# Kernel tuning notes

Measured on AMD Instinct MI355X. Metric: run time of the kernel, lower is better.

## Reference

```python
import jax, jax.numpy as jnp
import numpy as np

# Stand-in base model config (HF-style causal LM)
L, D, H, DFF, V, T = 2, 1024, 16, 4096, 32000, 2
HD = D // H
B, S = 2, 1024


def setup_inputs() -> dict:
    key = jax.random.key(0)
    ks = jax.random.split(key, 20)
    s = 0.02
    ds = 0.002  # task-vector deltas are small finetuning differences
    inp = {
        "input_ids": jax.random.randint(ks[0], (B, S), 0, V, dtype=jnp.int32),
        "labels": jax.random.randint(ks[1], (B, S), 0, V, dtype=jnp.int32),
        "lambdas": jax.random.uniform(ks[2], (T,), jnp.float32) * 0.5,
        # base parameters (frozen, like base_model)
        "emb": jax.random.normal(ks[3], (V, D), jnp.float32) * s,
        "Wqkv": jax.random.normal(ks[4], (L, D, 3 * D), jnp.float32) * s,
        "Wo": jax.random.normal(ks[5], (L, D, D), jnp.float32) * s,
        "W1": jax.random.normal(ks[6], (L, D, DFF), jnp.float32) * s,
        "W2": jax.random.normal(ks[7], (L, DFF, D), jnp.float32) * s,
        "g1": jnp.ones((L, D), jnp.float32),
        "g2": jnp.ones((L, D), jnp.float32),
        "gf": jnp.ones((D,), jnp.float32),
        # stacked task-vector deltas: leading dim T (one slice per CPUStoredTaskVector)
        "d_emb": jax.random.normal(ks[8], (T, V, D), jnp.float32) * ds,
        "d_Wqkv": jax.random.normal(ks[9], (T, L, D, 3 * D), jnp.float32) * ds,
        "d_Wo": jax.random.normal(ks[10], (T, L, D, D), jnp.float32) * ds,
        "d_W1": jax.random.normal(ks[11], (T, L, D, DFF), jnp.float32) * ds,
        "d_W2": jax.random.normal(ks[12], (T, L, DFF, D), jnp.float32) * ds,
        "d_g1": jax.random.normal(ks[13], (T, L, D), jnp.float32) * ds,
        "d_g2": jax.random.normal(ks[14], (T, L, D), jnp.float32) * ds,
        "d_gf": jax.random.normal(ks[15], (T, D), jnp.float32) * ds,
    }
    return inp


def _ln(x, g):
    mu = x.mean(-1, keepdims=True)
    var = ((x - mu) ** 2).mean(-1, keepdims=True)
    return (x - mu) * jax.lax.rsqrt(var + 1e-5) * g


def reference(input_ids, labels, lambdas, emb, Wqkv, Wo, W1, W2, g1, g2, gf,
              d_emb, d_Wqkv, d_Wo, d_W1, d_W2, d_g1, d_g2, d_gf):
    # fused layerwise merge: param + sum_i lambdas[i] * delta_i (single pass over all deltas)
    m = lambda base, d: base + jnp.einsum("t,t...->...", lambdas, d)
    emb_m = m(emb, d_emb)
    x = emb_m[input_ids]  # [B, S, D]
    b, s, _ = x.shape
    causal = jnp.tril(jnp.ones((s, s), bool))

    def body(h, p):
        wqkv, wo, w1, w2, gg1, gg2 = p
        a = _ln(h, gg1)
        qkv = a @ wqkv  # [B,S,3D]
        q, k, v = jnp.split(qkv, 3, axis=-1)
        q = q.reshape(b, s, H, HD)
        k = k.reshape(b, s, H, HD)
        v = v.reshape(b, s, H, HD)
        att = jnp.einsum("bqhd,bkhd->bhqk", q, k) / jnp.sqrt(jnp.float32(HD))
        att = jnp.where(causal, att, jnp.float32(-1e9))
        att = jax.nn.softmax(att, axis=-1)
        o = jnp.einsum("bhqk,bkhd->bqhd", att, v).reshape(b, s, D)
        h = h + o @ wo
        a = _ln(h, gg2)
        h = h + jax.nn.gelu(a @ w1) @ w2
        return h, None

    merged = (m(Wqkv, d_Wqkv), m(Wo, d_Wo), m(W1, d_W1), m(W2, d_W2),
              m(g1, d_g1), m(g2, d_g2))
    x, _ = jax.lax.scan(body, x, merged)
    x = _ln(x, m(gf, d_gf))
    logits = x @ emb_m.T  # tied embeddings, [B,S,V]
    # HF causal-LM loss: shift logits left, labels right
    logp = jax.nn.log_softmax(logits[:, :-1, :], axis=-1)
    tgt = labels[:, 1:]
    nll = -jnp.take_along_axis(logp, tgt[..., None].astype(jnp.int32), axis=-1)[..., 0]
    return nll.mean()
```

## Files before the change

### kernel.cpp

```cpp
#include <hip/hip_runtime.h>
#include <math.h>

#define L_ 2
#define D_ 1024
#define H_ 16
#define HD_ 64
#define DFF_ 4096
#define V_ 32000
#define B_ 2
#define S_ 1024
#define BS_ (B_*S_)
#define D3_ (3*D_)
#define VC_ 6400

typedef __attribute__((ext_vector_type(8))) short short8;
typedef __attribute__((ext_vector_type(4))) float f32x4;

__device__ __forceinline__ float b2f(unsigned short u) {
    return __uint_as_float(((unsigned int)u) << 16);
}
__device__ __forceinline__ unsigned short f2b(float f) {
    unsigned int u = __float_as_uint(f);
    return (unsigned short)((u + 0x7fffu + ((u >> 16) & 1u)) >> 16);
}
__device__ __forceinline__ float blo(unsigned int u) { return __uint_as_float(u << 16); }
__device__ __forceinline__ float bhi(unsigned int u) { return __uint_as_float(u & 0xffff0000u); }

__device__ __forceinline__ void gld16(const void* g, void* l) {
    __builtin_amdgcn_global_load_lds(
        (const __attribute__((address_space(1))) unsigned int*)g,
        (__attribute__((address_space(3))) unsigned int*)l, 16, 0, 0);
}


__global__ void merge_f32_kernel(const float* __restrict__ base, const float* __restrict__ dlt,
                                 size_t tstride, const float* __restrict__ lam,
                                 float* __restrict__ out, int n) {
    float l0 = lam[0], l1 = lam[1];
    for (int i = blockIdx.x * blockDim.x + threadIdx.x; i < n; i += gridDim.x * blockDim.x)
        out[i] = base[i] + l0 * dlt[i] + l1 * dlt[i + tstride];
}

__global__ void merge_bf16_kernel(const float* __restrict__ base, const float* __restrict__ dlt,
                                  size_t tstride, const float* __restrict__ lam,
                                  unsigned short* __restrict__ out, size_t n4) {
    float l0 = lam[0], l1 = lam[1];
    for (size_t q = blockIdx.x * blockDim.x + threadIdx.x; q < n4; q += (size_t)gridDim.x * blockDim.x) {
        size_t i = q * 4;
        float4 b = *(const float4*)(base + i);
        float4 d0 = *(const float4*)(dlt + i);
        float4 d1 = *(const float4*)(dlt + tstride + i);
        ushort4 o;
        o.x = f2b(b.x + l0 * d0.x + l1 * d1.x);
        o.y = f2b(b.y + l0 * d0.y + l1 * d1.y);
        o.z = f2b(b.z + l0 * d0.z + l1 * d1.z);
        o.w = f2b(b.w + l0 * d0.w + l1 * d1.w);
        *(ushort4*)(out + i) = o;
    }
}

__global__ __launch_bounds__(256) void mt_kernel(const float* __restrict__ in,
                                                 const float* __restrict__ din, size_t tstride,
                                                 const float* __restrict__ lam,
                                                 unsigned short* __restrict__ outT,
                                                 int K, int N) {
    __shared__ float T[64][65];
    float l0 = lam[0], l1 = lam[1];
    int n0 = blockIdx.x * 64, k0 = blockIdx.y * 64;
    int tr = threadIdx.x >> 4;
    int tc = threadIdx.x & 15;
    #pragma unroll
    for (int rep = 0; rep < 4; rep++) {
        int kk = tr + rep * 16;
        size_t idx = (size_t)(k0 + kk) * N + n0 + tc * 4;
        float4 b = *(const float4*)(in + idx);
        float4 d0 = *(const float4*)(din + idx);
        float4 d1 = *(const float4*)(din + tstride + idx);
        T[kk][tc * 4 + 0] = b.x + l0 * d0.x + l1 * d1.x;
        T[kk][tc * 4 + 1] = b.y + l0 * d0.y + l1 * d1.y;
        T[kk][tc * 4 + 2] = b.z + l0 * d0.z + l1 * d1.z;
        T[kk][tc * 4 + 3] = b.w + l0 * d0.w + l1 * d1.w;
    }
    __syncthreads();
    #pragma unroll
    for (int rep = 0; rep < 4; rep++) {
        int n = tr + rep * 16;
        int kc = tc * 4;
        ushort4 o;
        o.x = f2b(T[kc + 0][n]);
        o.y = f2b(T[kc + 1][n]);
        o.z = f2b(T[kc + 2][n]);
        o.w = f2b(T[kc + 3][n]);
        *(ushort4*)(outT + (size_t)(n0 + n) * K + k0 + kc) = o;
    }
}


__global__ void embed_kernel(const int* __restrict__ ids, const unsigned short* __restrict__ embm,
                             float* __restrict__ h) {
    int row = blockIdx.x;
    int id = ids[row];
    const unsigned short* src = embm + (size_t)id * D_;
    float* dst = h + (size_t)row * D_;
    for (int d = threadIdx.x; d < D_; d += 256) dst[d] = b2f(src[d]);
}

__global__ __launch_bounds__(256) void ln_kernel(const float* __restrict__ x,
                                                 const float* __restrict__ g,
                                                 unsigned short* __restrict__ out) {
    __shared__ float sred[8];
    int row = blockIdx.x;
    const float* xr = x + (size_t)row * D_;
    float s = 0.f, ss = 0.f;
    for (int d = threadIdx.x; d < D_; d += 256) { float v = xr[d]; s += v; ss += v * v; }
    for (int o = 32; o > 0; o >>= 1) { s += __shfl_down(s, o); ss += __shfl_down(ss, o); }
    int lane = threadIdx.x & 63, wid = threadIdx.x >> 6;
    if (lane == 0) { sred[wid] = s; sred[4 + wid] = ss; }
    __syncthreads();
    if (threadIdx.x == 0) {
        sred[0] = sred[0] + sred[1] + sred[2] + sred[3];
        sred[4] = sred[4] + sred[5] + sred[6] + sred[7];
    }
    __syncthreads();
    float mu = sred[0] * (1.0f / D_);
    float var = sred[4] * (1.0f / D_) - mu * mu;
    float r = rsqrtf(var + 1e-5f);
    unsigned short* orow = out + (size_t)row * D_;
    for (int d = threadIdx.x; d < D_; d += 256) orow[d] = f2b((xr[d] - mu) * r * g[d]);
}

template<int MODE>
__global__ __launch_bounds__(256) void gemm_mfma(const unsigned short* __restrict__ A,
                                                 const unsigned short* __restrict__ Bt,
                                                 float* __restrict__ Cf,
                                                 unsigned short* __restrict__ Cb,
                                                 int M, int N, int K) {
    __shared__ unsigned short As[128 * 32];
    __shared__ unsigned short Bs[128 * 32];
    int bm = blockIdx.y * 128, bn = blockIdx.x * 128;
    int tid = threadIdx.x;
    int w = tid >> 6, lane = tid & 63;
    int wm = (w & 1) * 64, wn = (w >> 1) * 64;
    int l15 = lane & 15, quad = lane >> 4;
    f32x4 acc[4][4] = {};

    int arow = w * 32 + (lane >> 2);
    int aseg = (lane & 3) * 8;
    const unsigned short* gA0 = A + (size_t)(bm + arow) * K + aseg;
    const unsigned short* gA1 = A + (size_t)(bm + arow + 16) * K + aseg;
    const unsigned short* gB0 = Bt + (size_t)(bn + arow) * K + aseg;
    const unsigned short* gB1 = Bt + (size_t)(bn + arow + 16) * K + aseg;
    unsigned short* lA0 = &As[arow * 32 + aseg];
    unsigned short* lA1 = &As[(arow + 16) * 32 + aseg];
    unsigned short* lB0 = &Bs[arow * 32 + aseg];
    unsigned short* lB1 = &Bs[(arow + 16) * 32 + aseg];

    for (int k0 = 0; k0 < K; k0 += 32) {
        gld16(gA0 + k0, lA0);
        gld16(gA1 + k0, lA1);
        gld16(gB0 + k0, lB0);
        gld16(gB1 + k0, lB1);
        __syncthreads();
        short8 af[4], bfm[4];
        #pragma unroll
        for (int i = 0; i < 4; i++) af[i] = *(const short8*)&As[(wm + i * 16 + l15) * 32 + quad * 8];
        #pragma unroll
        for (int j = 0; j < 4; j++) bfm[j] = *(const short8*)&Bs[(wn + j * 16 + l15) * 32 + quad * 8];
        #pragma unroll
        for (int i = 0; i < 4; i++)
            #pragma unroll
            for (int j = 0; j < 4; j++)
                acc[i][j] = __builtin_amdgcn_mfma_f32_16x16x32_bf16(af[i], bfm[j], acc[i][j], 0, 0, 0);
        __syncthreads();
    }

    #pragma unroll
    for (int i = 0; i < 4; i++) {
        int row = bm + wm + i * 16 + quad * 4;
        #pragma unroll
        for (int j = 0; j < 4; j++) {
            int col = bn + wn + j * 16 + l15;
            #pragma unroll
            for (int r = 0; r < 4; r++) {
                size_t idx = (size_t)(row + r) * N + col;
                float v = acc[i][j][r];
                if (MODE == 0) Cf[idx] = v;
                if (MODE == 1) Cf[idx] += v;
                if (MODE == 2) Cb[idx] = f2b(v);
                if (MODE == 3) {
                    float c = 0.7978845608028654f * (v + 0.044715f * v * v * v);
                    Cb[idx] = f2b(0.5f * v * (1.0f + tanhf(c)));
                }
            }
        }
    }
}

#define UNPACK8(u, dst) { (dst)[0]=blo((u).x);(dst)[1]=bhi((u).x);(dst)[2]=blo((u).y);(dst)[3]=bhi((u).y);(dst)[4]=blo((u).z);(dst)[5]=bhi((u).z);(dst)[6]=blo((u).w);(dst)[7]=bhi((u).w); }

__global__ __launch_bounds__(256) void attn_kernel(const unsigned short* __restrict__ qkv,
                                                   unsigned short* __restrict__ attno) {
    int qt = blockIdx.x, h = blockIdx.y, b = blockIdx.z;
    int tid = threadIdx.x;
    int tq = tid >> 4, tk = tid & 15;
    __shared__ float Qs[64][68];
    __shared__ float Kt[64][68];
    __shared__ float Vs[64][68];
    __shared__ unsigned short Ps[64][68];

    float o[4][4] = {};
    float m_i[4] = {-1e30f, -1e30f, -1e30f, -1e30f};
    float l_i[4] = {0.f, 0.f, 0.f, 0.f};

    int rr = tid >> 2, dseg = tid & 3, d0 = dseg * 16;

    {
        const unsigned short* g = qkv + (size_t)(b * S_ + qt * 64 + rr) * D3_ + h * HD_ + d0;
        uint4 u0 = *(const uint4*)g;
        uint4 u1 = *(const uint4*)(g + 8);
        float* qd = &Qs[rr][d0];
        UNPACK8(u0, qd); UNPACK8(u1, qd + 8);
    }

    for (int kt = 0; kt <= qt; kt++) {
        __syncthreads();
        {
            const unsigned short* g = qkv + (size_t)(b * S_ + kt * 64 + rr) * D3_ + h * HD_ + d0;
            uint4 ku0 = *(const uint4*)(g + D_);
            uint4 ku1 = *(const uint4*)(g + D_ + 8);
            uint4 vu0 = *(const uint4*)(g + 2 * D_);
            uint4 vu1 = *(const uint4*)(g + 2 * D_ + 8);
            float ktmp[16];
            UNPACK8(ku0, ktmp); UNPACK8(ku1, ktmp + 8);
            #pragma unroll
            for (int u = 0; u < 16; u++) Kt[d0 + u][rr] = ktmp[u];
            float* vd = &Vs[rr][d0];
            UNPACK8(vu0, vd); UNPACK8(vu1, vd + 8);
        }
        __syncthreads();

        float s[4][4] = {};
        for (int d = 0; d < 64; d++) {
            float4 kv = *(const float4*)&Kt[d][tk * 4];
            float q0 = Qs[tq * 4 + 0][d], q1 = Qs[tq * 4 + 1][d];
            float q2 = Qs[tq * 4 + 2][d], q3 = Qs[tq * 4 + 3][d];
            s[0][0] += q0 * kv.x; s[0][1] += q0 * kv.y; s[0][2] += q0 * kv.z; s[0][3] += q0 * kv.w;
            s[1][0] += q1 * kv.x; s[1][1] += q1 * kv.y; s[1][2] += q1 * kv.z; s[1][3] += q1 * kv.w;
            s[2][0] += q2 * kv.x; s[2][1] += q2 * kv.y; s[2][2] += q2 * kv.z; s[2][3] += q2 * kv.w;
            s[3][0] += q3 * kv.x; s[3][1] += q3 * kv.y; s[3][2] += q3 * kv.z; s[3][3] += q3 * kv.w;
        }
        #pragma unroll
        for (int i = 0; i < 4; i++)
            #pragma unroll
            for (int j = 0; j < 4; j++) {
                float v = s[i][j] * 0.125f;
                if (kt == qt && (tk * 4 + j) > (tq * 4 + i)) v = -1e30f;
                s[i][j] = v;
            }
        #pragma unroll
        for (int i = 0; i < 4; i++) {
            float rm = fmaxf(fmaxf(s[i][0], s[i][1]), fmaxf(s[i][2], s[i][3]));
            for (int off = 1; off < 16; off <<= 1) rm = fmaxf(rm, __shfl_xor(rm, off));
            float mnew = fmaxf(m_i[i], rm);
            float alpha = __expf(m_i[i] - mnew);
            float lsum = 0.f;
            ushort4 pb;
            {
                float p0 = __expf(s[i][0] - mnew), p1 = __expf(s[i][1] - mnew);
                float p2 = __expf(s[i][2] - mnew), p3 = __expf(s[i][3] - mnew);
                lsum = p0 + p1 + p2 + p3;
                pb.x = f2b(p0); pb.y = f2b(p1); pb.z = f2b(p2); pb.w = f2b(p3);
            }
            for (int off = 1; off < 16; off <<= 1) lsum += __shfl_xor(lsum, off);
            l_i[i] = l_i[i] * alpha + lsum;
            m_i[i] = mnew;
            #pragma unroll
            for (int j = 0; j < 4; j++) o[i][j] *= alpha;
            *(ushort4*)&Ps[tq * 4 + i][tk * 4] = pb;
        }
        __syncthreads();
        for (int k = 0; k < 64; k++) {
            float4 vv = *(const float4*)&Vs[k][tk * 4];
            float p0 = b2f(Ps[tq * 4 + 0][k]);
            float p1 = b2f(Ps[tq * 4 + 1][k]);
            float p2 = b2f(Ps[tq * 4 + 2][k]);
            float p3 = b2f(Ps[tq * 4 + 3][k]);
            o[0][0] += p0 * vv.x; o[0][1] += p0 * vv.y; o[0][2] += p0 * vv.z; o[0][3] += p0 * vv.w;
            o[1][0] += p1 * vv.x; o[1][1] += p1 * vv.y; o[1][2] += p1 * vv.z; o[1][3] += p1 * vv.w;
            o[2][0] += p2 * vv.x; o[2][1] += p2 * vv.y; o[2][2] += p2 * vv.z; o[2][3] += p2 * vv.w;
            o[3][0] += p3 * vv.x; o[3][1] += p3 * vv.y; o[3][2] += p3 * vv.z; o[3][3] += p3 * vv.w;
        }
    }

    #pragma unroll
    for (int i = 0; i < 4; i++) {
        float inv = 1.0f / l_i[i];
        size_t row = (size_t)(b * S_ + qt * 64 + tq * 4 + i);
        #pragma unroll
        for (int j = 0; j < 4; j++)
            attno[row * D_ + h * HD_ + tk * 4 + j] = f2b(o[i][j] * inv);
    }
}


__global__ void loss_init_kernel(float* rm, float* rl, float* rtl) {
    int i = blockIdx.x * blockDim.x + threadIdx.x;
    if (i < BS_) { rm[i] = -1e30f; rl[i] = 0.f; rtl[i] = 0.f; }
}

__global__ __launch_bounds__(256) void loss_chunk_kernel(const float* __restrict__ lg,
                                                         const int* __restrict__ labels,
                                                         float* rm, float* rl, float* rtl,
                                                         int v0) {
    int row = blockIdx.x;
    const float* lr = lg + (size_t)row * VC_;
    int tid = threadIdx.x;
    __shared__ float sred[8];
    float m = -1e30f;
    for (int j = tid; j < VC_; j += 256) m = fmaxf(m, lr[j]);
    for (int o = 32; o > 0; o >>= 1) m = fmaxf(m, __shfl_down(m, o));
    int lane = tid & 63, wid = tid >> 6;
    if (lane == 0) sred[wid] = m;
    __syncthreads();
    if (tid == 0) sred[0] = fmaxf(fmaxf(sred[0], sred[1]), fmaxf(sred[2], sred[3]));
    __syncthreads();
    float cm = sred[0];
    float s = 0.f;
    for (int j = tid; j < VC_; j += 256) s += __expf(lr[j] - cm);
    for (int o = 32; o > 0; o >>= 1) s += __shfl_down(s, o);
    if (lane == 0) sred[4 + wid] = s;
    __syncthreads();
    if (tid == 0) {
        float cs = sred[4] + sred[5] + sred[6] + sred[7];
        float om = rm[row], ol = rl[row];
        float nm = fmaxf(om, cm);
        rl[row] = ol * __expf(om - nm) + cs * __expf(cm - nm);
        rm[row] = nm;
        int b = row / S_, spos = row % S_;
        if (spos < S_ - 1) {
            int tgt = labels[b * S_ + spos + 1];
            if (tgt >= v0 && tgt < v0 + VC_) rtl[row] = lr[tgt - v0];
        }
    }
}

__global__ __launch_bounds__(256) void loss_final_kernel(const float* rm, const float* rl,
                                                         const float* rtl, float* out) {
    __shared__ float sred[4];
    float s = 0.f;
    for (int row = threadIdx.x; row < BS_; row += 256) {
        int spos = row % S_;
        if (spos < S_ - 1) s += (rm[row] + logf(rl[row])) - rtl[row];
    }
    for (int o = 32; o > 0; o >>= 1) s += __shfl_down(s, o);
    int lane = threadIdx.x & 63, wid = threadIdx.x >> 6;
    if (lane == 0) sred[wid] = s;
    __syncthreads();
    if (threadIdx.x == 0)
        out[0] = (sred[0] + sred[1] + sred[2] + sred[3]) * (1.0f / (B_ * (S_ - 1)));
}


extern "C" void kernel_launch(void* const* d_in, const int* in_sizes, int n_in,
                              void* d_out, int out_size, void* d_ws, size_t ws_size,
                              hipStream_t stream) {
    const int*   ids    = (const int*)d_in[0];
    const int*   labels = (const int*)d_in[1];
    const float* lam    = (const float*)d_in[2];
    const float* emb    = (const float*)d_in[3];
    const float* Wqkv   = (const float*)d_in[4];
    const float* Wo     = (const float*)d_in[5];
    const float* W1     = (const float*)d_in[6];
    const float* W2     = (const float*)d_in[7];
    const float* g1     = (const float*)d_in[8];
    const float* g2     = (const float*)d_in[9];
    const float* gf     = (const float*)d_in[10];
    const float* dEmb   = (const float*)d_in[11];
    const float* dWqkv  = (const float*)d_in[12];
    const float* dWo    = (const float*)d_in[13];
    const float* dW1    = (const float*)d_in[14];
    const float* dW2    = (const float*)d_in[15];
    const float* dG1    = (const float*)d_in[16];
    const float* dG2    = (const float*)d_in[17];
    const float* dGf    = (const float*)d_in[18];
    float* out = (float*)d_out;

    char* wsb = (char*)d_ws;
    size_t off = 0;
    auto alloc = [&](size_t bytes) {
        off = (off + 255) & ~(size_t)255;
        void* p = wsb + off;
        off += bytes;
        return p;
    };
    unsigned short* embm  = (unsigned short*)alloc((size_t)V_ * D_ * 2);
    unsigned short* WqkvT = (unsigned short*)alloc((size_t)L_ * D3_ * D_ * 2);
    unsigned short* WoT   = (unsigned short*)alloc((size_t)L_ * D_ * D_ * 2);
    unsigned short* W1T   = (unsigned short*)alloc((size_t)L_ * DFF_ * D_ * 2);
    unsigned short* W2T   = (unsigned short*)alloc((size_t)L_ * D_ * DFF_ * 2);
    float* g1m = (float*)alloc((size_t)L_ * D_ * 4);
    float* g2m = (float*)alloc((size_t)L_ * D_ * 4);
    float* gfm = (float*)alloc((size_t)D_ * 4);
    float* h   = (float*)alloc((size_t)BS_ * D_ * 4);
    unsigned short* a_bf  = (unsigned short*)alloc((size_t)BS_ * D_ * 2);
    unsigned short* qkv   = (unsigned short*)alloc((size_t)BS_ * D3_ * 2);
    unsigned short* attno = (unsigned short*)alloc((size_t)BS_ * D_ * 2);
    unsigned short* ffh   = (unsigned short*)alloc((size_t)BS_ * DFF_ * 2);
    float* lchunk = (float*)alloc((size_t)BS_ * VC_ * 4);
    float* rm  = (float*)alloc(BS_ * 4);
    float* rl  = (float*)alloc(BS_ * 4);
    float* rtl = (float*)alloc(BS_ * 4);

    merge_bf16_kernel<<<4096, 256, 0, stream>>>(emb, dEmb, (size_t)V_ * D_, lam, embm, (size_t)V_ * D_ / 4);
    for (int l = 0; l < L_; l++) {
        mt_kernel<<<dim3(D3_ / 64, D_ / 64), 256, 0, stream>>>(
            Wqkv + (size_t)l * D_ * D3_, dWqkv + (size_t)l * D_ * D3_, (size_t)L_ * D_ * D3_,
            lam, WqkvT + (size_t)l * D3_ * D_, D_, D3_);
        mt_kernel<<<dim3(D_ / 64, D_ / 64), 256, 0, stream>>>(
            Wo + (size_t)l * D_ * D_, dWo + (size_t)l * D_ * D_, (size_t)L_ * D_ * D_,
            lam, WoT + (size_t)l * D_ * D_, D_, D_);
        mt_kernel<<<dim3(DFF_ / 64, D_ / 64), 256, 0, stream>>>(
            W1 + (size_t)l * D_ * DFF_, dW1 + (size_t)l * D_ * DFF_, (size_t)L_ * D_ * DFF_,
            lam, W1T + (size_t)l * DFF_ * D_, D_, DFF_);
        mt_kernel<<<dim3(D_ / 64, DFF_ / 64), 256, 0, stream>>>(
            W2 + (size_t)l * DFF_ * D_, dW2 + (size_t)l * DFF_ * D_, (size_t)L_ * DFF_ * D_,
            lam, W2T + (size_t)l * D_ * DFF_, DFF_, D_);
    }
    merge_f32_kernel<<<8, 256, 0, stream>>>(g1, dG1, (size_t)L_ * D_, lam, g1m, L_ * D_);
    merge_f32_kernel<<<8, 256, 0, stream>>>(g2, dG2, (size_t)L_ * D_, lam, g2m, L_ * D_);
    merge_f32_kernel<<<4, 256, 0, stream>>>(gf, dGf, (size_t)D_, lam, gfm, D_);

    embed_kernel<<<BS_, 256, 0, stream>>>(ids, embm, h);

    for (int l = 0; l < L_; l++) {
        ln_kernel<<<BS_, 256, 0, stream>>>(h, g1m + l * D_, a_bf);
        gemm_mfma<2><<<dim3(D3_ / 128, BS_ / 128), 256, 0, stream>>>(
            a_bf, WqkvT + (size_t)l * D3_ * D_, nullptr, qkv, BS_, D3_, D_);
        attn_kernel<<<dim3(S_ / 64, H_, B_), 256, 0, stream>>>(qkv, attno);
        gemm_mfma<1><<<dim3(D_ / 128, BS_ / 128), 256, 0, stream>>>(
            attno, WoT + (size_t)l * D_ * D_, h, nullptr, BS_, D_, D_);
        ln_kernel<<<BS_, 256, 0, stream>>>(h, g2m + l * D_, a_bf);
        gemm_mfma<3><<<dim3(DFF_ / 128, BS_ / 128), 256, 0, stream>>>(
            a_bf, W1T + (size_t)l * DFF_ * D_, nullptr, ffh, BS_, DFF_, D_);
        gemm_mfma<1><<<dim3(D_ / 128, BS_ / 128), 256, 0, stream>>>(
            ffh, W2T + (size_t)l * D_ * DFF_, h, nullptr, BS_, D_, DFF_);
    }

    ln_kernel<<<BS_, 256, 0, stream>>>(h, gfm, a_bf);

    loss_init_kernel<<<(BS_ + 255) / 256, 256, 0, stream>>>(rm, rl, rtl);
    for (int c = 0; c < V_ / VC_; c++) {
        int v0 = c * VC_;
        gemm_mfma<0><<<dim3(VC_ / 128, BS_ / 128), 256, 0, stream>>>(
            a_bf, embm + (size_t)v0 * D_, lchunk, nullptr, BS_, VC_, D_);
        loss_chunk_kernel<<<BS_, 256, 0, stream>>>(lchunk, labels, rm, rl, rtl, v0);
    }
    loss_final_kernel<<<1, 256, 0, stream>>>(rm, rl, rtl, out);
}
```

Before: 1.794 ms.

## Rewrite attention kernel to use bf16 MFMA for QK and PV

Replaces the scalar FMA attention inner loops with 16x16x32 bf16 MFMA instructions. Each wavefront now owns 16 query rows, with Q held in registers and K kept as bf16 in shared memory. V is stored transposed as float in LDS and repacked into bf16 pairs before the PV MFMA. The aim is to cut the ALU-bound attention cost; it adds per-wave P staging through LDS and a more intricate fragment layout that must match the MFMA lane mapping.

```diff
diff --git a/kernel.cpp b/kernel.cpp
--- a/kernel.cpp
+++ b/kernel.cpp
@@ -15,6 +15,7 @@
 
 typedef __attribute__((ext_vector_type(8))) short short8;
 typedef __attribute__((ext_vector_type(4))) float f32x4;
+typedef __attribute__((ext_vector_type(4))) unsigned int uint4v;
 
 __device__ __forceinline__ float b2f(unsigned short u) {
     return __uint_as_float(((unsigned int)u) << 16);
@@ -202,103 +203,120 @@
                                                    unsigned short* __restrict__ attno) {
     int qt = blockIdx.x, h = blockIdx.y, b = blockIdx.z;
     int tid = threadIdx.x;
-    int tq = tid >> 4, tk = tid & 15;
-    __shared__ float Qs[64][68];
-    __shared__ float Kt[64][68];
-    __shared__ float Vs[64][68];
-    __shared__ unsigned short Ps[64][68];
-
-    float o[4][4] = {};
+    int w = tid >> 6, lane = tid & 63;
+    int l15 = lane & 15, quad = lane >> 4;
+
+    __shared__ unsigned short Ks[64][72];
+    __shared__ float Vt[64][68];
+    __shared__ unsigned short Ps[4][16][72];
+
+    short8 aq[2];
+    {
+        const unsigned short* gq = qkv + (size_t)(b * S_ + qt * 64 + w * 16 + l15) * D3_ + h * HD_ + quad * 8;
+        aq[0] = *(const short8*)(gq);
+        aq[1] = *(const short8*)(gq + 32);
+    }
+
+    f32x4 oacc[4] = {};
     float m_i[4] = {-1e30f, -1e30f, -1e30f, -1e30f};
     float l_i[4] = {0.f, 0.f, 0.f, 0.f};
 
-    int rr = tid >> 2, dseg = tid & 3, d0 = dseg * 16;
-
-    {
-        const unsigned short* g = qkv + (size_t)(b * S_ + qt * 64 + rr) * D3_ + h * HD_ + d0;
-        uint4 u0 = *(const uint4*)g;
-        uint4 u1 = *(const uint4*)(g + 8);
-        float* qd = &Qs[rr][d0];
-        UNPACK8(u0, qd); UNPACK8(u1, qd + 8);
-    }
+    int krr = tid >> 3, kseg = tid & 7;
+    int vrr = tid >> 2, vd0 = (tid & 3) * 16;
 
     for (int kt = 0; kt <= qt; kt++) {
         __syncthreads();
         {
-            const unsigned short* g = qkv + (size_t)(b * S_ + kt * 64 + rr) * D3_ + h * HD_ + d0;
-            uint4 ku0 = *(const uint4*)(g + D_);
-            uint4 ku1 = *(const uint4*)(g + D_ + 8);
-            uint4 vu0 = *(const uint4*)(g + 2 * D_);
-            uint4 vu1 = *(const uint4*)(g + 2 * D_ + 8);
-            float ktmp[16];
-            UNPACK8(ku0, ktmp); UNPACK8(ku1, ktmp + 8);
-            #pragma unroll
-            for (int u = 0; u < 16; u++) Kt[d0 + u][rr] = ktmp[u];
-            float* vd = &Vs[rr][d0];
-            UNPACK8(vu0, vd); UNPACK8(vu1, vd + 8);
+            const unsigned short* gk = qkv + (size_t)(b * S_ + kt * 64 + krr) * D3_ + D_ + h * HD_ + kseg * 8;
+            uint4 u0 = *(const uint4*)gk;
+            uint4 u1 = *(const uint4*)(gk + (size_t)32 * D3_);
+            *(uint4*)&Ks[krr][kseg * 8] = u0;
+            *(uint4*)&Ks[krr + 32][kseg * 8] = u1;
+        }
+        {
+            const unsigned short* gv = qkv + (size_t)(b * S_ + kt * 64 + vrr) * D3_ + 2 * D_ + h * HD_ + vd0;
+            uint4 v0 = *(const uint4*)gv;
+            uint4 v1 = *(const uint4*)(gv + 8);
+            float tmp[16];
+            UNPACK8(v0, tmp); UNPACK8(v1, tmp + 8);
+            #pragma unroll
+            for (int u = 0; u < 16; u++) Vt[vd0 + u][vrr] = tmp[u];
         }
         __syncthreads();
 
-        float s[4][4] = {};
-        for (int d = 0; d < 64; d++) {
-            float4 kv = *(const float4*)&Kt[d][tk * 4];
-            float q0 = Qs[tq * 4 + 0][d], q1 = Qs[tq * 4 + 1][d];
-            float q2 = Qs[tq * 4 + 2][d], q3 = Qs[tq * 4 + 3][d];
-            s[0][0] += q0 * kv.x; s[0][1] += q0 * kv.y; s[0][2] += q0 * kv.z; s[0][3] += q0 * kv.w;
-            s[1][0] += q1 * kv.x; s[1][1] += q1 * kv.y; s[1][2] += q1 * kv.z; s[1][3] += q1 * kv.w;
-            s[2][0] += q2 * kv.x; s[2][1] += q2 * kv.y; s[2][2] += q2 * kv.z; s[2][3] += q2 * kv.w;
-            s[3][0] += q3 * kv.x; s[3][1] += q3 * kv.y; s[3][2] += q3 * kv.z; s[3][3] += q3 * kv.w;
-        }
-        #pragma unroll
-        for (int i = 0; i < 4; i++)
+        f32x4 sc[4] = {};
+        #pragma unroll
+        for (int kk = 0; kk < 2; kk++)
             #pragma unroll
             for (int j = 0; j < 4; j++) {
-                float v = s[i][j] * 0.125f;
-                if (kt == qt && (tk * 4 + j) > (tq * 4 + i)) v = -1e30f;
-                s[i][j] = v;
+                short8 bk = *(const short8*)&Ks[j * 16 + l15][kk * 32 + quad * 8];
+                sc[j] = __builtin_amdgcn_mfma_f32_16x16x32_bf16(aq[kk], bk, sc[j], 0, 0, 0);
             }
-        #pragma unroll
-        for (int i = 0; i < 4; i++) {
-            float rm = fmaxf(fmaxf(s[i][0], s[i][1]), fmaxf(s[i][2], s[i][3]));
-            for (int off = 1; off < 16; off <<= 1) rm = fmaxf(rm, __shfl_xor(rm, off));
-            float mnew = fmaxf(m_i[i], rm);
-            float alpha = __expf(m_i[i] - mnew);
-            float lsum = 0.f;
-            ushort4 pb;
-            {
-                float p0 = __expf(s[i][0] - mnew), p1 = __expf(s[i][1] - mnew);
-                float p2 = __expf(s[i][2] - mnew), p3 = __expf(s[i][3] - mnew);
-                lsum = p0 + p1 + p2 + p3;
-                pb.x = f2b(p0); pb.y = f2b(p1); pb.z = f2b(p2); pb.w = f2b(p3);
+
+        bool diag = (kt == qt);
+        #pragma unroll
+        for (int j = 0; j < 4; j++)
+            #pragma unroll
+            for (int r = 0; r < 4; r++) {
+                float v = sc[j][r] * 0.125f;
+                if (diag && (j * 16 + l15) > (w * 16 + quad * 4 + r)) v = -1e30f;
+                sc[j][r] = v;
             }
-            for (int off = 1; off < 16; off <<= 1) lsum += __shfl_xor(lsum, off);
-            l_i[i] = l_i[i] * alpha + lsum;
-            m_i[i] = mnew;
-            #pragma unroll
-            for (int j = 0; j < 4; j++) o[i][j] *= alpha;
-            *(ushort4*)&Ps[tq * 4 + i][tk * 4] = pb;
-        }
-        __syncthreads();
-        for (int k = 0; k < 64; k++) {
-            float4 vv = *(const float4*)&Vs[k][tk * 4];
-            float p0 = b2f(Ps[tq * 4 + 0][k]);
-            float p1 = b2f(Ps[tq * 4 + 1][k]);
-            float p2 = b2f(Ps[tq * 4 + 2][k]);
-            float p3 = b2f(Ps[tq * 4 + 3][k]);
-            o[0][0] += p0 * vv.x; o[0][1] += p0 * vv.y; o[0][2] += p0 * vv.z; o[0][3] += p0 * vv.w;
-            o[1][0] += p1 * vv.x; o[1][1] += p1 * vv.y; o[1][2] += p1 * vv.z; o[1][3] += p1 * vv.w;
-            o[2][0] += p2 * vv.x; o[2][1] += p2 * vv.y; o[2][2] += p2 * vv.z; o[2][3] += p2 * vv.w;
-            o[3][0] += p3 * vv.x; o[3][1] += p3 * vv.y; o[3][2] += p3 * vv.z; o[3][3] += p3 * vv.w;
+
+        #pragma unroll
+        for (int r = 0; r < 4; r++) {
+            float rm = fmaxf(fmaxf(sc[0][r], sc[1][r]), fmaxf(sc[2][r], sc[3][r]));
+            rm = fmaxf(rm, __shfl_xor(rm, 1));
+            rm = fmaxf(rm, __shfl_xor(rm, 2));
+            rm = fmaxf(rm, __shfl_xor(rm, 4));
+            rm = fmaxf(rm, __shfl_xor(rm, 8));
+            float mnew = fmaxf(m_i[r], rm);
+            float alpha = __expf(m_i[r] - mnew);
+            float p0 = __expf(sc[0][r] - mnew);
+            float p1 = __expf(sc[1][r] - mnew);
+            float p2 = __expf(sc[2][r] - mnew);
+            float p3 = __expf(sc[3][r] - mnew);
+            float ls = p0 + p1 + p2 + p3;
+            ls += __shfl_xor(ls, 1);
+            ls += __shfl_xor(ls, 2);
+            ls += __shfl_xor(ls, 4);
+            ls += __shfl_xor(ls, 8);
+            l_i[r] = l_i[r] * alpha + ls;
+            m_i[r] = mnew;
+            oacc[0][r] *= alpha; oacc[1][r] *= alpha;
+            oacc[2][r] *= alpha; oacc[3][r] *= alpha;
+            Ps[w][quad * 4 + r][ 0 + l15] = f2b(p0);
+            Ps[w][quad * 4 + r][16 + l15] = f2b(p1);
+            Ps[w][quad * 4 + r][32 + l15] = f2b(p2);
+            Ps[w][quad * 4 + r][48 + l15] = f2b(p3);
+        }
+
+        #pragma unroll
+        for (int kk = 0; kk < 2; kk++) {
+            short8 pa = *(const short8*)&Ps[w][l15][kk * 32 + quad * 8];
+            #pragma unroll
+            for (int j = 0; j < 4; j++) {
+                const float* vp = &Vt[j * 16 + l15][kk * 32 + quad * 8];
+                f32x4 f0 = *(const f32x4*)vp;
+                f32x4 f1 = *(const f32x4*)(vp + 4);
+                unsigned int b0 = (__float_as_uint(f0[1]) & 0xffff0000u) | (__float_as_uint(f0[0]) >> 16);
+                unsigned int b1 = (__float_as_uint(f0[3]) & 0xffff0000u) | (__float_as_uint(f0[2]) >> 16);
+                unsigned int b2 = (__float_as_uint(f1[1]) & 0xffff0000u) | (__float_as_uint(f1[0]) >> 16);
+                unsigned int b3 = (__float_as_uint(f1[3]) & 0xffff0000u) | (__float_as_uint(f1[2]) >> 16);
+                union { uint4v u; short8 s; } cvt;
+                cvt.u = (uint4v){b0, b1, b2, b3};
+                oacc[j] = __builtin_amdgcn_mfma_f32_16x16x32_bf16(pa, cvt.s, oacc[j], 0, 0, 0);
+            }
         }
     }
 
     #pragma unroll
-    for (int i = 0; i < 4; i++) {
-        float inv = 1.0f / l_i[i];
-        size_t row = (size_t)(b * S_ + qt * 64 + tq * 4 + i);
+    for (int r = 0; r < 4; r++) {
+        float inv = 1.0f / l_i[r];
+        size_t row = (size_t)(b * S_ + qt * 64 + w * 16 + quad * 4 + r);
         #pragma unroll
         for (int j = 0; j < 4; j++)
-            attno[row * D_ + h * HD_ + tk * 4 + j] = f2b(o[i][j] * inv);
+            attno[row * D_ + h * HD_ + j * 16 + l15] = f2b(oacc[j][r] * inv);
     }
 }
 
```

New measurement: 1.615 ms. 1.11x faster.
